# Kernel optimization log

Measured on AMD Instinct MI355X. Metric: run time of the kernel, lower is better.

Reference implementation:

```python
import jax, jax.numpy as jnp
import numpy as np

B, T, W, L, H, TW = 2, 4096, 2048, 2048, 8, 4
HD = L // H  # head dim for block-diagonal gate projections


def setup_inputs() -> dict:
    key = jax.random.key(0)
    ks = jax.random.split(key, 16)
    inv_sqrt_w = 1.0 / np.sqrt(W)
    inv_sqrt_l = 1.0 / np.sqrt(L)
    inv_sqrt_hd = 1.0 / np.sqrt(HD)
    return {
        "x": jax.random.normal(ks[0], (B, T, W), dtype=jnp.float32),
        "segment_pos": jnp.tile(jnp.arange(T, dtype=jnp.int32), (B, 1)),
        # linear_y, linear_x: width -> lru_width
        "w_y": jax.random.normal(ks[1], (W, L), dtype=jnp.float32) * inv_sqrt_w,
        "b_y": jnp.zeros((L,), dtype=jnp.float32),
        "w_x": jax.random.normal(ks[2], (W, L), dtype=jnp.float32) * inv_sqrt_w,
        "b_x": jnp.zeros((L,), dtype=jnp.float32),
        # linear_out: lru_width -> width
        "w_out": jax.random.normal(ks[3], (L, W), dtype=jnp.float32) * inv_sqrt_l,
        "b_out": jnp.zeros((W,), dtype=jnp.float32),
        # depthwise causal temporal conv, kernel [TW, L]
        "conv_w": jax.random.normal(ks[4], (TW, L), dtype=jnp.float32) / np.sqrt(TW),
        "conv_b": jnp.zeros((L,), dtype=jnp.float32),
        # RG-LRU: a_param and two block-diagonal gate projections
        "a_param": jax.random.uniform(ks[5], (L,), dtype=jnp.float32, minval=-2.0, maxval=1.0),
        "igate_w": jax.random.normal(ks[6], (H, HD, HD), dtype=jnp.float32) * inv_sqrt_hd,
        "igate_b": jnp.zeros((H, HD), dtype=jnp.float32),
        "agate_w": jax.random.normal(ks[7], (H, HD, HD), dtype=jnp.float32) * inv_sqrt_hd,
        "agate_b": jnp.zeros((H, HD), dtype=jnp.float32),
    }


def _block_diag_linear(u, w, b):
    # u: [B,T,L] -> [B,T,H,HD] blockwise projected -> [B,T,L]
    uh = u.reshape(u.shape[0], u.shape[1], H, HD)
    y = jnp.einsum("bthd,hde->bthe", uh, w) + b
    return y.reshape(u.shape)


def _forward(x, segment_pos, w_y, b_y, w_x, b_x, w_out, b_out,
             conv_w, conv_b, a_param, igate_w, igate_b, agate_w, agate_b):
    # gate branch: linear_y + tanh-approx GELU
    y = jax.nn.gelu(jnp.einsum("btw,wl->btl", x, w_y) + b_y, approximate=True)
    # recurrent branch: linear_x
    xb = jnp.einsum("btw,wl->btl", x, w_x) + b_x
    # causal depthwise temporal conv (width TW), zero history before t=0
    x_pad = jnp.pad(xb, ((0, 0), (TW - 1, 0), (0, 0)))
    conv = conv_b + sum(conv_w[j] * x_pad[:, j:j + T] for j in range(TW))
    # RG-LRU gates
    gate_x = jax.nn.sigmoid(_block_diag_linear(conv, igate_w, igate_b))
    gate_a = jax.nn.sigmoid(_block_diag_linear(conv, agate_w, agate_b))
    log_a = -8.0 * gate_a * jax.nn.softplus(a_param)  # [B,T,L]
    a = jnp.exp(log_a)
    reset = (segment_pos == 0)[..., None]  # [B,T,1]
    multiplier = jnp.sqrt(1.0 - jnp.exp(2.0 * log_a))
    multiplier = jnp.where(reset, 1.0, multiplier)
    normed = conv * gate_x * multiplier
    a_masked = jnp.where(reset, 0.0, a)
    # diagonal linear recurrence: h_t = a_t * h_{t-1} + normed_t
    def step(h, inp):
        a_t, x_t = inp
        h = a_t * h + x_t
        return h, h
    h0 = jnp.zeros((x.shape[0], L), dtype=x.dtype)
    _, hs = jax.lax.scan(step, h0, (a_masked.transpose(1, 0, 2), normed.transpose(1, 0, 2)))
    hs = hs.transpose(1, 0, 2)  # [B,T,L]
    # elementwise gate then output projection
    return jnp.einsum("btl,lw->btw", hs * y, w_out) + b_out


def reference(x, segment_pos, w_y, b_y, w_x, b_x, w_out, b_out,
              conv_w, conv_b, a_param, igate_w, igate_b, agate_w, agate_b):
    return _forward(x, segment_pos, w_y, b_y, w_x, b_x, w_out, b_out,
                    conv_w, conv_b, a_param, igate_w, igate_b, agate_w, agate_b)
```

## Files before the change

kernel.cpp:

```cpp
#include <hip/hip_runtime.h>
#include <cstdint>
#include <math.h>

typedef _Float16 f16;
typedef f16 f16x8 __attribute__((ext_vector_type(8)));
typedef f16 f16x4 __attribute__((ext_vector_type(4)));
typedef float f32x4 __attribute__((ext_vector_type(4)));

#define BATCH 2
#define TSEQ 4096
#define WID 2048
#define LRU 2048
#define NHEAD 8
#define HDIM 256
#define MTOT (BATCH * TSEQ)
#define CT 64
#define NC (TSEQ / CT)

__device__ __forceinline__ void gl2lds16(const f16* g, f16* l) {
  __builtin_amdgcn_global_load_lds(
      (__attribute__((address_space(1))) uint32_t*)(uintptr_t)g,
      (__attribute__((address_space(3))) uint32_t*)(uint32_t)(uintptr_t)l,
      16, 0, 0);
}

__device__ __forceinline__ float sigmoidf_(float x) { return 1.f / (1.f + expf(-x)); }
__device__ __forceinline__ float f16bits_to_f(uint32_t b) {
  return (float)__builtin_bit_cast(f16, (uint16_t)b);
}

__global__ void cast_f32_f16_kernel(const float* __restrict__ in, f16* __restrict__ out, int n4) {
  int i = blockIdx.x * 256 + threadIdx.x;
  if (i >= n4) return;
  float4 v = ((const float4*)in)[i];
  f16x4 o = { (f16)v.x, (f16)v.y, (f16)v.z, (f16)v.w };
  ((f16x4*)out)[i] = o;
}

__global__ void transpose_cast_kernel(const float* __restrict__ in, f16* __restrict__ out,
                                      int R, int C, long long inStride, long long outStride) {
  __shared__ float tile[32][33];
  const float* ib = in + (long long)blockIdx.z * inStride;
  f16* ob = out + (long long)blockIdx.z * outStride;
  int c0 = blockIdx.x * 32, r0 = blockIdx.y * 32;
  int tx = threadIdx.x, ty = threadIdx.y;
#pragma unroll
  for (int i = 0; i < 32; i += 8)
    tile[ty + i][tx] = ib[(long long)(r0 + ty + i) * C + c0 + tx];
  __syncthreads();
#pragma unroll
  for (int i = 0; i < 32; i += 8)
    ob[(long long)(c0 + ty + i) * R + r0 + tx] = (f16)tile[tx][ty + i];
}

__global__ __launch_bounds__(256, 2) void gemm_dual(
    const f16* __restrict__ A, const f16* __restrict__ B1T, const f16* __restrict__ B2T,
    const float* __restrict__ b1, const float* __restrict__ b2,
    f16* __restrict__ Y, f16* __restrict__ X2, int M, int N, int K) {
  __shared__ __align__(16) f16 As[128 * 32];
  __shared__ __align__(16) f16 B1s[128 * 32];
  __shared__ __align__(16) f16 B2s[128 * 32];
  const int m0 = blockIdx.x * 128, n0 = blockIdx.y * 128;
  const int t = threadIdx.x;
  const int lane = t & 63, wave = t >> 6;
  const int wr = (wave >> 1) * 64, wc = (wave & 1) * 64;
  const int l15 = lane & 15, quad = lane >> 4;
  const int srow = t >> 2, scol = (t & 3) * 8;

  const f16* Ag = A + (long long)(m0 + srow) * K + scol;
  const f16* B1g = B1T + (long long)(n0 + srow) * K + scol;
  const f16* B2g = B2T + (long long)(n0 + srow) * K + scol;

  f32x4 c1[4][4] = {};
  f32x4 c2[4][4] = {};
  for (int k0 = 0; k0 < K; k0 += 32) {
    gl2lds16(Ag, &As[t * 8]);   gl2lds16(Ag + (long long)64 * K, &As[64 * 32 + t * 8]);
    gl2lds16(B1g, &B1s[t * 8]); gl2lds16(B1g + (long long)64 * K, &B1s[64 * 32 + t * 8]);
    gl2lds16(B2g, &B2s[t * 8]); gl2lds16(B2g + (long long)64 * K, &B2s[64 * 32 + t * 8]);
    Ag += 32; B1g += 32; B2g += 32;
    __syncthreads();
    f16x8 af[4], b1f[4], b2f[4];
#pragma unroll
    for (int i = 0; i < 4; ++i)
      af[i] = *(const f16x8*)&As[(wr + i * 16 + l15) * 32 + quad * 8];
#pragma unroll
    for (int j = 0; j < 4; ++j) {
      b1f[j] = *(const f16x8*)&B1s[(wc + j * 16 + l15) * 32 + quad * 8];
      b2f[j] = *(const f16x8*)&B2s[(wc + j * 16 + l15) * 32 + quad * 8];
    }
#pragma unroll
    for (int i = 0; i < 4; ++i)
#pragma unroll
      for (int j = 0; j < 4; ++j) {
        c1[i][j] = __builtin_amdgcn_mfma_f32_16x16x32_f16(af[i], b1f[j], c1[i][j], 0, 0, 0);
        c2[i][j] = __builtin_amdgcn_mfma_f32_16x16x32_f16(af[i], b2f[j], c2[i][j], 0, 0, 0);
      }
    __syncthreads();
  }
#pragma unroll
  for (int i = 0; i < 4; ++i) {
#pragma unroll
    for (int j = 0; j < 4; ++j) {
      const int col = n0 + wc + j * 16 + l15;
      const float b1v = b1[col], b2v = b2[col];
      const int row0 = m0 + wr + i * 16 + quad * 4;
#pragma unroll
      for (int r = 0; r < 4; ++r) {
        long long off = (long long)(row0 + r) * N + col;
        float v = c1[i][j][r] + b1v;
        float u = v + 0.044715f * v * v * v;
        float g = 0.5f * v * (1.f + tanhf(0.7978845608028654f * u));
        Y[off] = (f16)g;
        X2[off] = (f16)(c2[i][j][r] + b2v);
      }
    }
  }
}

__global__ __launch_bounds__(256, 2) void gemm_bt(
    const f16* __restrict__ A, const f16* __restrict__ BT, const float* __restrict__ bias,
    float* __restrict__ Cf, int M, int N, int K) {
  __shared__ __align__(16) f16 As[128 * 32];
  __shared__ __align__(16) f16 Bs[128 * 32];
  const int m0 = blockIdx.x * 128, n0 = blockIdx.y * 128;
  const int t = threadIdx.x;
  const int lane = t & 63, wave = t >> 6;
  const int wr = (wave >> 1) * 64, wc = (wave & 1) * 64;
  const int l15 = lane & 15, quad = lane >> 4;
  const int srow = t >> 2, scol = (t & 3) * 8;

  const f16* Ag = A + (long long)(m0 + srow) * K + scol;
  const f16* Bg = BT + (long long)(n0 + srow) * K + scol;

  f32x4 acc[4][4] = {};
  for (int k0 = 0; k0 < K; k0 += 32) {
    gl2lds16(Ag, &As[t * 8]); gl2lds16(Ag + (long long)64 * K, &As[64 * 32 + t * 8]);
    gl2lds16(Bg, &Bs[t * 8]); gl2lds16(Bg + (long long)64 * K, &Bs[64 * 32 + t * 8]);
    Ag += 32; Bg += 32;
    __syncthreads();
    f16x8 af[4], bf[4];
#pragma unroll
    for (int i = 0; i < 4; ++i)
      af[i] = *(const f16x8*)&As[(wr + i * 16 + l15) * 32 + quad * 8];
#pragma unroll
    for (int j = 0; j < 4; ++j)
      bf[j] = *(const f16x8*)&Bs[(wc + j * 16 + l15) * 32 + quad * 8];
#pragma unroll
    for (int i = 0; i < 4; ++i)
#pragma unroll
      for (int j = 0; j < 4; ++j)
        acc[i][j] = __builtin_amdgcn_mfma_f32_16x16x32_f16(af[i], bf[j], acc[i][j], 0, 0, 0);
    __syncthreads();
  }
#pragma unroll
  for (int i = 0; i < 4; ++i) {
#pragma unroll
    for (int j = 0; j < 4; ++j) {
      const int col = n0 + wc + j * 16 + l15;
      const float bv = bias[col];
      const int row0 = m0 + wr + i * 16 + quad * 4;
#pragma unroll
      for (int r = 0; r < 4; ++r)
        Cf[(long long)(row0 + r) * N + col] = acc[i][j][r] + bv;
    }
  }
}

__global__ void conv_kernel(const f16* __restrict__ xb, const float* __restrict__ cw,
                            const float* __restrict__ cb, f16* __restrict__ convh) {
  int l = threadIdx.x * 8;
  int m = blockIdx.x;
  int tpos = m & (TSEQ - 1);
  float acc[8];
  {
    float4 c0 = *(const float4*)&cb[l];
    float4 c1 = *(const float4*)&cb[l + 4];
    acc[0] = c0.x; acc[1] = c0.y; acc[2] = c0.z; acc[3] = c0.w;
    acc[4] = c1.x; acc[5] = c1.y; acc[6] = c1.z; acc[7] = c1.w;
  }
#pragma unroll
  for (int d = 0; d < 4; ++d) {
    if (tpos >= d) {
      f16x8 xv = *(const f16x8*)&xb[(long long)(m - d) * LRU + l];
      float4 w0 = *(const float4*)&cw[(3 - d) * LRU + l];
      float4 w1 = *(const float4*)&cw[(3 - d) * LRU + l + 4];
      acc[0] += w0.x * (float)xv[0]; acc[1] += w0.y * (float)xv[1];
      acc[2] += w0.z * (float)xv[2]; acc[3] += w0.w * (float)xv[3];
      acc[4] += w1.x * (float)xv[4]; acc[5] += w1.y * (float)xv[5];
      acc[6] += w1.z * (float)xv[6]; acc[7] += w1.w * (float)xv[7];
    }
  }
  f16x8 o;
#pragma unroll
  for (int k = 0; k < 8; ++k) o[k] = (f16)acc[k];
  *(f16x8*)&convh[(long long)m * LRU + l] = o;
}

__global__ __launch_bounds__(256, 2) void gates_kernel(
    const f16* __restrict__ Ah, const f16* __restrict__ BiT, const f16* __restrict__ BaT,
    const float* __restrict__ ib, const float* __restrict__ ab,
    const float* __restrict__ a_param, const int* __restrict__ segpos,
    uint32_t* __restrict__ AN) {
  __shared__ __align__(16) f16 As[128 * 32];
  __shared__ __align__(16) f16 Bi[128 * 32];
  __shared__ __align__(16) f16 Ba[128 * 32];
  const int m0 = blockIdx.x * 128;
  const int h = blockIdx.y >> 1;
  const int ncol0 = h * HDIM + (blockIdx.y & 1) * 128;
  const int t = threadIdx.x;
  const int lane = t & 63, wave = t >> 6;
  const int wr = (wave >> 1) * 64, wc = (wave & 1) * 64;
  const int l15 = lane & 15, quad = lane >> 4;
  const int srow = t >> 2, scol = (t & 3) * 8;

  const f16* Ag = Ah + (long long)(m0 + srow) * LRU + h * HDIM + scol;
  const f16* Big = BiT + (long long)(ncol0 + srow) * HDIM + scol;
  const f16* Bag = BaT + (long long)(ncol0 + srow) * HDIM + scol;

  f32x4 ci[4][4] = {};
  f32x4 ca[4][4] = {};
  for (int k0 = 0; k0 < HDIM; k0 += 32) {
    gl2lds16(Ag, &As[t * 8]);  gl2lds16(Ag + (long long)64 * LRU, &As[64 * 32 + t * 8]);
    gl2lds16(Big, &Bi[t * 8]); gl2lds16(Big + 64 * HDIM, &Bi[64 * 32 + t * 8]);
    gl2lds16(Bag, &Ba[t * 8]); gl2lds16(Bag + 64 * HDIM, &Ba[64 * 32 + t * 8]);
    Ag += 32; Big += 32; Bag += 32;
    __syncthreads();
    f16x8 af[4], bif[4], baf[4];
#pragma unroll
    for (int i = 0; i < 4; ++i)
      af[i] = *(const f16x8*)&As[(wr + i * 16 + l15) * 32 + quad * 8];
#pragma unroll
    for (int j = 0; j < 4; ++j) {
      bif[j] = *(const f16x8*)&Bi[(wc + j * 16 + l15) * 32 + quad * 8];
      baf[j] = *(const f16x8*)&Ba[(wc + j * 16 + l15) * 32 + quad * 8];
    }
#pragma unroll
    for (int i = 0; i < 4; ++i)
#pragma unroll
      for (int j = 0; j < 4; ++j) {
        ci[i][j] = __builtin_amdgcn_mfma_f32_16x16x32_f16(af[i], bif[j], ci[i][j], 0, 0, 0);
        ca[i][j] = __builtin_amdgcn_mfma_f32_16x16x32_f16(af[i], baf[j], ca[i][j], 0, 0, 0);
      }
    __syncthreads();
  }
#pragma unroll
  for (int i = 0; i < 4; ++i) {
#pragma unroll
    for (int j = 0; j < 4; ++j) {
      const int col = ncol0 + wc + j * 16 + l15;
      const float ibv = ib[col], abv = ab[col];
      const float sp = log1pf(expf(a_param[col]));
      const int row0 = m0 + wr + i * 16 + quad * 4;
#pragma unroll
      for (int r = 0; r < 4; ++r) {
        const int row = row0 + r;
        float gx = sigmoidf_(ci[i][j][r] + ibv);
        float ga = sigmoidf_(ca[i][j][r] + abv);
        float la = -8.f * ga * sp;
        bool rs = (segpos[row] == 0);
        float a = rs ? 0.f : expf(la);
        float mult = rs ? 1.f : sqrtf(fmaxf(1.f - expf(2.f * la), 0.f));
        float cv = (float)Ah[(long long)row * LRU + col];
        uint32_t afx = __float2uint_rn(a * 65536.f);
        if (afx > 65535u) afx = 65535u;
        f16 nh = (f16)(cv * gx * mult);
        AN[(long long)row * LRU + col] =
            afx | ((uint32_t)__builtin_bit_cast(uint16_t, nh) << 16);
      }
    }
  }
}

__global__ void scan1_kernel(const uint32_t* __restrict__ AN,
                             float* __restrict__ Ac, float* __restrict__ Hc) {
  int l = blockIdx.x * 256 + threadIdx.x;
  int c = blockIdx.y, b = blockIdx.z;
  long long base = ((long long)b * TSEQ + (long long)c * CT) * LRU + l;
  float A = 1.f, hv = 0.f;
#pragma unroll 8
  for (int s = 0; s < CT; ++s) {
    uint32_t p = AN[base + (long long)s * LRU];
    float a = (float)(p & 0xFFFFu) * (1.f / 65536.f);
    float x = f16bits_to_f(p >> 16);
    A *= a;
    hv = a * hv + x;
  }
  int o = (b * NC + c) * LRU + l;
  Ac[o] = A;
  Hc[o] = hv;
}

__global__ void scan2_kernel(const float* __restrict__ Ac, const float* __restrict__ Hc,
                             float* __restrict__ P) {
  int l = blockIdx.x * 256 + threadIdx.x;
  int b = blockIdx.y;
  float hv = 0.f;
#pragma unroll 8
  for (int c = 0; c < NC; ++c) {
    int o = (b * NC + c) * LRU + l;
    P[o] = hv;
    hv = Ac[o] * hv + Hc[o];
  }
}

__global__ void scan3_kernel(const uint32_t* __restrict__ AN,
                             const float* __restrict__ P, const f16* __restrict__ Yh,
                             f16* __restrict__ G) {
  int l = blockIdx.x * 256 + threadIdx.x;
  int c = blockIdx.y, b = blockIdx.z;
  long long base = ((long long)b * TSEQ + (long long)c * CT) * LRU + l;
  float hv = P[(b * NC + c) * LRU + l];
#pragma unroll 4
  for (int s = 0; s < CT; ++s) {
    long long o = base + (long long)s * LRU;
    uint32_t p = AN[o];
    float a = (float)(p & 0xFFFFu) * (1.f / 65536.f);
    float x = f16bits_to_f(p >> 16);
    hv = a * hv + x;
    G[o] = (f16)(hv * (float)Yh[o]);
  }
}

extern "C" void kernel_launch(void* const* d_in, const int* in_sizes, int n_in,
                              void* d_out, int out_size, void* d_ws, size_t ws_size,
                              hipStream_t stream) {
  (void)in_sizes; (void)n_in; (void)out_size; (void)ws_size;
  const float* x          = (const float*)d_in[0];
  const int*   segment_pos= (const int*)d_in[1];
  const float* w_y        = (const float*)d_in[2];
  const float* b_y        = (const float*)d_in[3];
  const float* w_x        = (const float*)d_in[4];
  const float* b_x        = (const float*)d_in[5];
  const float* w_out      = (const float*)d_in[6];
  const float* b_out      = (const float*)d_in[7];
  const float* conv_w     = (const float*)d_in[8];
  const float* conv_b     = (const float*)d_in[9];
  const float* a_param    = (const float*)d_in[10];
  const float* igate_w    = (const float*)d_in[11];
  const float* igate_b    = (const float*)d_in[12];
  const float* agate_w    = (const float*)d_in[13];
  const float* agate_b    = (const float*)d_in[14];
  float* out = (float*)d_out;

  char* base = (char*)d_ws;
  size_t off = 0;
  auto alloc = [&](size_t nbytes) -> void* {
    void* p = base + off;
    off = (off + nbytes + 255) & ~(size_t)255;
    return p;
  };
  f16*     Xh    = (f16*)alloc((size_t)MTOT * LRU * 2);
  f16*     Yh    = (f16*)alloc((size_t)MTOT * LRU * 2);
  f16*     XBh   = (f16*)alloc((size_t)MTOT * LRU * 2);
  f16*     convh = (f16*)alloc((size_t)MTOT * LRU * 2);
  uint32_t* AN   = (uint32_t*)alloc((size_t)MTOT * LRU * 4);
  f16*     wyT   = (f16*)alloc((size_t)WID * LRU * 2);
  f16*     wxT   = (f16*)alloc((size_t)WID * LRU * 2);
  f16*     woutT = (f16*)alloc((size_t)LRU * WID * 2);
  f16*     igwT  = (f16*)alloc((size_t)NHEAD * HDIM * HDIM * 2);
  f16*     agwT  = (f16*)alloc((size_t)NHEAD * HDIM * HDIM * 2);
  float*   Ac    = (float*)alloc((size_t)BATCH * NC * LRU * 4);
  float*   Hc    = (float*)alloc((size_t)BATCH * NC * LRU * 4);
  float*   Pc    = (float*)alloc((size_t)BATCH * NC * LRU * 4);
  f16*     G     = Xh;

  dim3 tb32(32, 8);
  cast_f32_f16_kernel<<<(MTOT * LRU / 4 + 255) / 256, 256, 0, stream>>>(x, Xh, MTOT * LRU / 4);
  transpose_cast_kernel<<<dim3(LRU / 32, WID / 32, 1), tb32, 0, stream>>>(w_y, wyT, WID, LRU, 0, 0);
  transpose_cast_kernel<<<dim3(LRU / 32, WID / 32, 1), tb32, 0, stream>>>(w_x, wxT, WID, LRU, 0, 0);
  transpose_cast_kernel<<<dim3(WID / 32, LRU / 32, 1), tb32, 0, stream>>>(w_out, woutT, LRU, WID, 0, 0);
  transpose_cast_kernel<<<dim3(HDIM / 32, HDIM / 32, NHEAD), tb32, 0, stream>>>(
      igate_w, igwT, HDIM, HDIM, (long long)HDIM * HDIM, (long long)HDIM * HDIM);
  transpose_cast_kernel<<<dim3(HDIM / 32, HDIM / 32, NHEAD), tb32, 0, stream>>>(
      agate_w, agwT, HDIM, HDIM, (long long)HDIM * HDIM, (long long)HDIM * HDIM);
  gemm_dual<<<dim3(MTOT / 128, LRU / 128), 256, 0, stream>>>(
      Xh, wyT, wxT, b_y, b_x, Yh, XBh, MTOT, LRU, WID);
  conv_kernel<<<MTOT, 256, 0, stream>>>(XBh, conv_w, conv_b, convh);
  gates_kernel<<<dim3(MTOT / 128, 2 * NHEAD), 256, 0, stream>>>(
      convh, igwT, agwT, igate_b, agate_b, a_param, segment_pos, AN);
  scan1_kernel<<<dim3(LRU / 256, NC, BATCH), 256, 0, stream>>>(AN, Ac, Hc);
  scan2_kernel<<<dim3(LRU / 256, BATCH), 256, 0, stream>>>(Ac, Hc, Pc);
  scan3_kernel<<<dim3(LRU / 256, NC, BATCH), 256, 0, stream>>>(AN, Pc, Yh, G);
  gemm_bt<<<dim3(MTOT / 128, WID / 128), 256, 0, stream>>>(G, woutT, b_out, out, MTOT, WID, LRU);
}
```

Before: 601.7 us.

## Fuse conv and chunk-scan stage into gates kernel, merge weight transposes

The depthwise causal conv now runs inside the gate-projection kernel. Each block computes its 128x256 conv tile directly into a swizzled LDS buffer, so the convh buffer no longer makes a global round trip. The per-chunk scan reduction (scan1) also moves into the gates epilogue, using cross-lane shuffles and an LDS carry between the wave rows, and the chunk length changes to 128 to match the block's M tile. The five weight transpose launches become two. The cost is 64KB of LDS per block, which may lower occupancy, and the conv work is repeated for both column halves of each head.

```diff
diff --git a/kernel.cpp b/kernel.cpp
--- a/kernel.cpp
+++ b/kernel.cpp
@@ -14,7 +14,7 @@
 #define NHEAD 8
 #define HDIM 256
 #define MTOT (BATCH * TSEQ)
-#define CT 64
+#define CT 128
 #define NC (TSEQ / CT)
 
 __device__ __forceinline__ void gl2lds16(const f16* g, f16* l) {
@@ -37,11 +37,13 @@
   ((f16x4*)out)[i] = o;
 }
 
-__global__ void transpose_cast_kernel(const float* __restrict__ in, f16* __restrict__ out,
-                                      int R, int C, long long inStride, long long outStride) {
+__global__ void transpose_big_kernel(const float* __restrict__ s0, const float* __restrict__ s1,
+                                     const float* __restrict__ s2, f16* __restrict__ d0,
+                                     f16* __restrict__ d1, f16* __restrict__ d2) {
   __shared__ float tile[32][33];
-  const float* ib = in + (long long)blockIdx.z * inStride;
-  f16* ob = out + (long long)blockIdx.z * outStride;
+  const int R = 2048, C = 2048;
+  const float* ib = blockIdx.z == 0 ? s0 : (blockIdx.z == 1 ? s1 : s2);
+  f16* ob = blockIdx.z == 0 ? d0 : (blockIdx.z == 1 ? d1 : d2);
   int c0 = blockIdx.x * 32, r0 = blockIdx.y * 32;
   int tx = threadIdx.x, ty = threadIdx.y;
 #pragma unroll
@@ -51,6 +53,23 @@
 #pragma unroll
   for (int i = 0; i < 32; i += 8)
     ob[(long long)(c0 + ty + i) * R + r0 + tx] = (f16)tile[tx][ty + i];
+}
+
+__global__ void transpose_small_kernel(const float* __restrict__ ig, const float* __restrict__ ag,
+                                       f16* __restrict__ igT, f16* __restrict__ agT) {
+  __shared__ float tile[32][33];
+  int z = blockIdx.z;
+  const float* ib = (z < 8 ? ig : ag) + (long long)(z & 7) * HDIM * HDIM;
+  f16* ob = (z < 8 ? igT : agT) + (long long)(z & 7) * HDIM * HDIM;
+  int c0 = blockIdx.x * 32, r0 = blockIdx.y * 32;
+  int tx = threadIdx.x, ty = threadIdx.y;
+#pragma unroll
+  for (int i = 0; i < 32; i += 8)
+    tile[ty + i][tx] = ib[(r0 + ty + i) * HDIM + c0 + tx];
+  __syncthreads();
+#pragma unroll
+  for (int i = 0; i < 32; i += 8)
+    ob[(c0 + ty + i) * HDIM + r0 + tx] = (f16)tile[tx][ty + i];
 }
 
 __global__ __launch_bounds__(256, 2) void gemm_dual(
@@ -166,69 +185,75 @@
   }
 }
 
-__global__ void conv_kernel(const f16* __restrict__ xb, const float* __restrict__ cw,
-                            const float* __restrict__ cb, f16* __restrict__ convh) {
-  int l = threadIdx.x * 8;
-  int m = blockIdx.x;
-  int tpos = m & (TSEQ - 1);
-  float acc[8];
-  {
-    float4 c0 = *(const float4*)&cb[l];
-    float4 c1 = *(const float4*)&cb[l + 4];
-    acc[0] = c0.x; acc[1] = c0.y; acc[2] = c0.z; acc[3] = c0.w;
-    acc[4] = c1.x; acc[5] = c1.y; acc[6] = c1.z; acc[7] = c1.w;
-  }
-#pragma unroll
-  for (int d = 0; d < 4; ++d) {
-    if (tpos >= d) {
-      f16x8 xv = *(const f16x8*)&xb[(long long)(m - d) * LRU + l];
-      float4 w0 = *(const float4*)&cw[(3 - d) * LRU + l];
-      float4 w1 = *(const float4*)&cw[(3 - d) * LRU + l + 4];
-      acc[0] += w0.x * (float)xv[0]; acc[1] += w0.y * (float)xv[1];
-      acc[2] += w0.z * (float)xv[2]; acc[3] += w0.w * (float)xv[3];
-      acc[4] += w1.x * (float)xv[4]; acc[5] += w1.y * (float)xv[5];
-      acc[6] += w1.z * (float)xv[6]; acc[7] += w1.w * (float)xv[7];
-    }
-  }
-  f16x8 o;
-#pragma unroll
-  for (int k = 0; k < 8; ++k) o[k] = (f16)acc[k];
-  *(f16x8*)&convh[(long long)m * LRU + l] = o;
-}
-
-__global__ __launch_bounds__(256, 2) void gates_kernel(
-    const f16* __restrict__ Ah, const f16* __restrict__ BiT, const f16* __restrict__ BaT,
+__global__ __launch_bounds__(256, 2) void gates_fused(
+    const f16* __restrict__ XBh, const float* __restrict__ cw, const float* __restrict__ cb,
+    const f16* __restrict__ BiT, const f16* __restrict__ BaT,
     const float* __restrict__ ib, const float* __restrict__ ab,
     const float* __restrict__ a_param, const int* __restrict__ segpos,
-    uint32_t* __restrict__ AN) {
-  __shared__ __align__(16) f16 As[128 * 32];
+    uint32_t* __restrict__ AN, float* __restrict__ Ac, float* __restrict__ Hc) {
+  __shared__ __align__(16) f16 As[128 * 256];
   __shared__ __align__(16) f16 Bi[128 * 32];
   __shared__ __align__(16) f16 Ba[128 * 32];
   const int m0 = blockIdx.x * 128;
   const int h = blockIdx.y >> 1;
-  const int ncol0 = h * HDIM + (blockIdx.y & 1) * 128;
+  const int half = blockIdx.y & 1;
+  const int ncol0 = h * HDIM + half * 128;
   const int t = threadIdx.x;
   const int lane = t & 63, wave = t >> 6;
   const int wr = (wave >> 1) * 64, wc = (wave & 1) * 64;
   const int l15 = lane & 15, quad = lane >> 4;
+
+#pragma unroll 4
+  for (int it = 0; it < 16; ++it) {
+    int idx = it * 256 + t;
+    int r = idx >> 5, kc = idx & 31;
+    int m = m0 + r, tpos = m & (TSEQ - 1);
+    int colbase = h * HDIM + kc * 8;
+    float acc[8];
+    {
+      float4 c0 = *(const float4*)&cb[colbase];
+      float4 c1 = *(const float4*)&cb[colbase + 4];
+      acc[0] = c0.x; acc[1] = c0.y; acc[2] = c0.z; acc[3] = c0.w;
+      acc[4] = c1.x; acc[5] = c1.y; acc[6] = c1.z; acc[7] = c1.w;
+    }
+#pragma unroll
+    for (int d = 0; d < 4; ++d) {
+      if (tpos >= d) {
+        f16x8 xv = *(const f16x8*)&XBh[(long long)(m - d) * LRU + colbase];
+        float4 w0 = *(const float4*)&cw[(3 - d) * LRU + colbase];
+        float4 w1 = *(const float4*)&cw[(3 - d) * LRU + colbase + 4];
+        acc[0] += w0.x * (float)xv[0]; acc[1] += w0.y * (float)xv[1];
+        acc[2] += w0.z * (float)xv[2]; acc[3] += w0.w * (float)xv[3];
+        acc[4] += w1.x * (float)xv[4]; acc[5] += w1.y * (float)xv[5];
+        acc[6] += w1.z * (float)xv[6]; acc[7] += w1.w * (float)xv[7];
+      }
+    }
+    f16x8 o;
+#pragma unroll
+    for (int k = 0; k < 8; ++k) o[k] = (f16)acc[k];
+    int gs = (kc & ~7) | ((kc ^ r) & 7);
+    *(f16x8*)&As[r * 256 + gs * 8] = o;
+  }
+  __syncthreads();
+
   const int srow = t >> 2, scol = (t & 3) * 8;
-
-  const f16* Ag = Ah + (long long)(m0 + srow) * LRU + h * HDIM + scol;
   const f16* Big = BiT + (long long)(ncol0 + srow) * HDIM + scol;
   const f16* Bag = BaT + (long long)(ncol0 + srow) * HDIM + scol;
-
   f32x4 ci[4][4] = {};
   f32x4 ca[4][4] = {};
   for (int k0 = 0; k0 < HDIM; k0 += 32) {
-    gl2lds16(Ag, &As[t * 8]);  gl2lds16(Ag + (long long)64 * LRU, &As[64 * 32 + t * 8]);
     gl2lds16(Big, &Bi[t * 8]); gl2lds16(Big + 64 * HDIM, &Bi[64 * 32 + t * 8]);
     gl2lds16(Bag, &Ba[t * 8]); gl2lds16(Bag + 64 * HDIM, &Ba[64 * 32 + t * 8]);
-    Ag += 32; Big += 32; Bag += 32;
+    Big += 32; Bag += 32;
     __syncthreads();
     f16x8 af[4], bif[4], baf[4];
 #pragma unroll
-    for (int i = 0; i < 4; ++i)
-      af[i] = *(const f16x8*)&As[(wr + i * 16 + l15) * 32 + quad * 8];
+    for (int i = 0; i < 4; ++i) {
+      int row = wr + i * 16 + l15;
+      int g = (k0 >> 3) + quad;
+      int gsw = (g & ~7) | ((g ^ row) & 7);
+      af[i] = *(const f16x8*)&As[row * 256 + gsw * 8];
+    }
 #pragma unroll
     for (int j = 0; j < 4; ++j) {
       bif[j] = *(const f16x8*)&Bi[(wc + j * 16 + l15) * 32 + quad * 8];
@@ -243,51 +268,85 @@
       }
     __syncthreads();
   }
-#pragma unroll
-  for (int i = 0; i < 4; ++i) {
-#pragma unroll
-    for (int j = 0; j < 4; ++j) {
-      const int col = ncol0 + wc + j * 16 + l15;
-      const float ibv = ib[col], abv = ab[col];
-      const float sp = log1pf(expf(a_param[col]));
-      const int row0 = m0 + wr + i * 16 + quad * 4;
+
+  const int mb = m0 >> 12;
+  const int cch = (m0 & (TSEQ - 1)) >> 7;
+  float Aw[4], hw[4];
+#pragma unroll
+  for (int j = 0; j < 4; ++j) {
+    const int cl = wc + j * 16 + l15;
+    const int col = ncol0 + cl;
+    const float ibv = ib[col], abv = ab[col];
+    const float sp = log1pf(expf(a_param[col]));
+    float A4[4], h4[4];
+#pragma unroll
+    for (int i = 0; i < 4; ++i) {
+      float Aseg = 1.f, hseg = 0.f;
 #pragma unroll
       for (int r = 0; r < 4; ++r) {
-        const int row = row0 + r;
+        const int rowL = wr + i * 16 + quad * 4 + r;
+        const int row = m0 + rowL;
         float gx = sigmoidf_(ci[i][j][r] + ibv);
         float ga = sigmoidf_(ca[i][j][r] + abv);
         float la = -8.f * ga * sp;
         bool rs = (segpos[row] == 0);
         float a = rs ? 0.f : expf(la);
-        float mult = rs ? 1.f : sqrtf(fmaxf(1.f - expf(2.f * la), 0.f));
-        float cv = (float)Ah[(long long)row * LRU + col];
         uint32_t afx = __float2uint_rn(a * 65536.f);
         if (afx > 65535u) afx = 65535u;
+        float aq = (float)afx * (1.f / 65536.f);
+        int cfull = half * 128 + cl;
+        int g = cfull >> 3, e = cfull & 7;
+        int gsw = (g & ~7) | ((g ^ rowL) & 7);
+        float cv = (float)As[rowL * 256 + gsw * 8 + e];
+        float mult = rs ? 1.f : sqrtf(fmaxf(1.f - aq * aq, 0.f));
         f16 nh = (f16)(cv * gx * mult);
         AN[(long long)row * LRU + col] =
             afx | ((uint32_t)__builtin_bit_cast(uint16_t, nh) << 16);
-      }
-    }
-  }
-}
-
-__global__ void scan1_kernel(const uint32_t* __restrict__ AN,
-                             float* __restrict__ Ac, float* __restrict__ Hc) {
-  int l = blockIdx.x * 256 + threadIdx.x;
-  int c = blockIdx.y, b = blockIdx.z;
-  long long base = ((long long)b * TSEQ + (long long)c * CT) * LRU + l;
-  float A = 1.f, hv = 0.f;
-#pragma unroll 8
-  for (int s = 0; s < CT; ++s) {
-    uint32_t p = AN[base + (long long)s * LRU];
-    float a = (float)(p & 0xFFFFu) * (1.f / 65536.f);
-    float x = f16bits_to_f(p >> 16);
-    A *= a;
-    hv = a * hv + x;
-  }
-  int o = (b * NC + c) * LRU + l;
-  Ac[o] = A;
-  Hc[o] = hv;
+        float xq = (float)nh;
+        hseg = aq * hseg + xq;
+        Aseg *= aq;
+      }
+      A4[i] = Aseg; h4[i] = hseg;
+    }
+#pragma unroll
+    for (int i = 0; i < 4; ++i) {
+      float A = A4[i], hv = h4[i];
+#pragma unroll
+      for (int d = 1; d <= 2; d <<= 1) {
+        int src = quad >= d ? lane - 16 * d : lane;
+        float Ap = __shfl(A, src);
+        float hp = __shfl(hv, src);
+        if (quad >= d) { hv = A * hp + hv; A = Ap * A; }
+      }
+      A4[i] = __shfl(A, 48 + l15);
+      h4[i] = __shfl(hv, 48 + l15);
+    }
+    float Awv = 1.f, hwv = 0.f;
+#pragma unroll
+    for (int i = 0; i < 4; ++i) { hwv = A4[i] * hwv + h4[i]; Awv *= A4[i]; }
+    Aw[j] = Awv; hw[j] = hwv;
+  }
+  float* carry = (float*)Bi;
+  __syncthreads();
+  if (wr == 0 && quad == 0) {
+#pragma unroll
+    for (int j = 0; j < 4; ++j) {
+      int cl = wc + j * 16 + l15;
+      carry[cl * 2] = Aw[j]; carry[cl * 2 + 1] = hw[j];
+    }
+  }
+  __syncthreads();
+  if (wr == 64 && quad == 0) {
+#pragma unroll
+    for (int j = 0; j < 4; ++j) {
+      int cl = wc + j * 16 + l15;
+      float At = carry[cl * 2], ht = carry[cl * 2 + 1];
+      float A = At * Aw[j];
+      float hv = Aw[j] * ht + hw[j];
+      int o = (mb * NC + cch) * LRU + ncol0 + cl;
+      Ac[o] = A; Hc[o] = hv;
+    }
+  }
 }
 
 __global__ void scan2_kernel(const float* __restrict__ Ac, const float* __restrict__ Hc,
@@ -352,7 +411,6 @@
   f16*     Xh    = (f16*)alloc((size_t)MTOT * LRU * 2);
   f16*     Yh    = (f16*)alloc((size_t)MTOT * LRU * 2);
   f16*     XBh   = (f16*)alloc((size_t)MTOT * LRU * 2);
-  f16*     convh = (f16*)alloc((size_t)MTOT * LRU * 2);
   uint32_t* AN   = (uint32_t*)alloc((size_t)MTOT * LRU * 4);
   f16*     wyT   = (f16*)alloc((size_t)WID * LRU * 2);
   f16*     wxT   = (f16*)alloc((size_t)WID * LRU * 2);
@@ -366,19 +424,12 @@
 
   dim3 tb32(32, 8);
   cast_f32_f16_kernel<<<(MTOT * LRU / 4 + 255) / 256, 256, 0, stream>>>(x, Xh, MTOT * LRU / 4);
-  transpose_cast_kernel<<<dim3(LRU / 32, WID / 32, 1), tb32, 0, stream>>>(w_y, wyT, WID, LRU, 0, 0);
-  transpose_cast_kernel<<<dim3(LRU / 32, WID / 32, 1), tb32, 0, stream>>>(w_x, wxT, WID, LRU, 0, 0);
-  transpose_cast_kernel<<<dim3(WID / 32, LRU / 32, 1), tb32, 0, stream>>>(w_out, woutT, LRU, WID, 0, 0);
-  transpose_cast_kernel<<<dim3(HDIM / 32, HDIM / 32, NHEAD), tb32, 0, stream>>>(
-      igate_w, igwT, HDIM, HDIM, (long long)HDIM * HDIM, (long long)HDIM * HDIM);
-  transpose_cast_kernel<<<dim3(HDIM / 32, HDIM / 32, NHEAD), tb32, 0, stream>>>(
-      agate_w, agwT, HDIM, HDIM, (long long)HDIM * HDIM, (long long)HDIM * HDIM);
+  transpose_big_kernel<<<dim3(64, 64, 3), tb32, 0, stream>>>(w_y, w_x, w_out, wyT, wxT, woutT);
+  transpose_small_kernel<<<dim3(8, 8, 16), tb32, 0, stream>>>(igate_w, agate_w, igwT, agwT);
   gemm_dual<<<dim3(MTOT / 128, LRU / 128), 256, 0, stream>>>(
       Xh, wyT, wxT, b_y, b_x, Yh, XBh, MTOT, LRU, WID);
-  conv_kernel<<<MTOT, 256, 0, stream>>>(XBh, conv_w, conv_b, convh);
-  gates_kernel<<<dim3(MTOT / 128, 2 * NHEAD), 256, 0, stream>>>(
-      convh, igwT, agwT, igate_b, agate_b, a_param, segment_pos, AN);
-  scan1_kernel<<<dim3(LRU / 256, NC, BATCH), 256, 0, stream>>>(AN, Ac, Hc);
+  gates_fused<<<dim3(MTOT / 128, 2 * NHEAD), 256, 0, stream>>>(
+      XBh, conv_w, conv_b, igwT, agwT, igate_b, agate_b, a_param, segment_pos, AN, Ac, Hc);
   scan2_kernel<<<dim3(LRU / 256, BATCH), 256, 0, stream>>>(Ac, Hc, Pc);
   scan3_kernel<<<dim3(LRU / 256, NC, BATCH), 256, 0, stream>>>(AN, Pc, Yh, G);
   gemm_bt<<<dim3(MTOT / 128, WID / 128), 256, 0, stream>>>(G, woutT, b_out, out, MTOT, WID, LRU);
```

Result: faster. 573.2 us (-4.7%).
